# Optimization experiments

Measured on AMD Instinct MI355X. Metric: run time of the kernel, lower is better.

Reference implementation:

```python
import jax, jax.numpy as jnp
import numpy as np

VOCAB = 4823          # round(feature_size_criteo[512])
EMB = 128             # embedding_size
B = 16384             # batch
N_SPARSE = 26
N_DENSE = 13
HID = 256


def setup_inputs() -> dict:
    key = jax.random.key(0)
    ks = jax.random.split(key, 8)
    dense_input = jax.random.normal(ks[0], (B, N_DENSE), dtype=jnp.float32)
    sparse_input = jax.random.randint(ks[1], (B, N_SPARSE), 0, VOCAB, dtype=jnp.int32)
    emb1 = jax.random.normal(ks[2], (VOCAB, 1), dtype=jnp.float32) * 0.02
    emb2 = jax.random.normal(ks[3], (VOCAB, EMB), dtype=jnp.float32) * 0.02
    fm_w = jax.random.normal(ks[4], (1, N_DENSE), dtype=jnp.float32) * 0.1
    w1 = jax.random.normal(ks[5], (HID, N_SPARSE * EMB), dtype=jnp.float32) * (1.0 / np.sqrt(N_SPARSE * EMB))
    w2 = jax.random.normal(ks[6], (HID, HID), dtype=jnp.float32) * (1.0 / np.sqrt(HID))
    w3 = jax.random.normal(ks[7], (1, HID), dtype=jnp.float32) * (1.0 / np.sqrt(HID))
    return {"dense_input": dense_input, "sparse_input": sparse_input,
            "emb1": emb1, "emb2": emb2, "fm_w": fm_w,
            "w1": w1, "w2": w2, "w3": w3}


def reference(dense_input, sparse_input, emb1, emb2, fm_w, w1, w2, w3):
    # first-order FM part
    sparse_1dim = emb1[sparse_input]                     # [B, 26, 1]
    fm_dense = dense_input @ fm_w.T                      # [B, 1]
    fm_sparse = jnp.sum(sparse_1dim, axis=1)             # [B, 1]
    y1 = fm_dense + fm_sparse

    # second-order FM part (sum-square minus square-sum trick)
    sparse_2dim = emb2[sparse_input]                     # [B, 26, EMB]
    s = jnp.sum(sparse_2dim, axis=1)                     # [B, EMB]
    ss = jnp.sum(jnp.square(sparse_2dim), axis=1)        # [B, EMB]
    y2 = 0.5 * jnp.sum(jnp.square(s) - ss, axis=1, keepdims=True)  # [B, 1]

    # deep MLP part
    flat = sparse_2dim.reshape(-1, N_SPARSE * EMB)       # [B, 26*EMB]
    h = jax.nn.relu(flat @ w1.T)
    h = jax.nn.relu(h @ w2.T)
    y3 = h @ w3.T                                        # [B, 1]

    return jax.nn.sigmoid(y1 + y2 + y3)
```

## Files before the change

### kernel.cpp

```cpp
#include <hip/hip_runtime.h>
#include <cstdint>
#include <cstddef>


#define B_ROWS   16384
#define NSPARSE  26
#define NDENSE   13
#define EMBD     128
#define HID      256
#define K1       (NSPARSE*EMBD)
#define VOCAB    4823
#define PAD_V    4864
#define NP       (NSPARSE*HID)

typedef unsigned short ushort_t;
typedef __attribute__((ext_vector_type(8))) short bf16x8;
typedef __attribute__((ext_vector_type(8))) unsigned short ushort8;
typedef __attribute__((ext_vector_type(4))) float f32x4;

__device__ __forceinline__ ushort_t f32_bf16(float x) {
    unsigned u = __builtin_bit_cast(unsigned, x);
    u += 0x7fffu + ((u >> 16) & 1u);
    return (ushort_t)(u >> 16);
}
__device__ __forceinline__ float bf16_f32(ushort_t h) {
    return __builtin_bit_cast(float, ((unsigned)h) << 16);
}

__device__ __forceinline__ void gl2lds16(const void* g, void* l) {
    __builtin_amdgcn_global_load_lds(
        (const __attribute__((address_space(1))) void*)g,
        (__attribute__((address_space(3))) void*)l, 16, 0, 0);
}

__global__ void split_kernel(const float* __restrict__ src,
                             ushort_t* __restrict__ dst, int n4) {
    int i = blockIdx.x * blockDim.x + threadIdx.x;
    if (i >= n4) return;
    float4 x = ((const float4*)src)[i];
    union { ushort_t u[4]; uint2 v; } H;
    float xs[4] = {x.x, x.y, x.z, x.w};
#pragma unroll
    for (int j = 0; j < 4; ++j) H.u[j] = f32_bf16(xs[j]);
    ((uint2*)dst)[i] = H.v;
}

__global__ void splitT_kernel(const float* __restrict__ w1,
                              ushort_t* __restrict__ dst, int n4) {
    int i = blockIdx.x * blockDim.x + threadIdx.x;
    if (i >= n4) return;
    int c    = i & 31;
    int rowp = i >> 5;
    int f = rowp >> 8, h = rowp & 255;
    float4 x = ((const float4*)w1)[h * (K1 / 4) + f * 32 + c];
    union { ushort_t u[4]; uint2 v; } H;
    float xs[4] = {x.x, x.y, x.z, x.w};
#pragma unroll
    for (int j = 0; j < 4; ++j) H.u[j] = f32_bf16(xs[j]);
    ((uint2*)dst)[i] = H.v;
}

template <int KDIM, bool RELU>
__global__ __launch_bounds__(256) void gemm_bf16_kernel(
    const ushort_t* __restrict__ A, const ushort_t* __restrict__ Bm,
    ushort_t* __restrict__ C, int ldc) {
    constexpr int NT = KDIM / 32;
    __shared__ union {
        ushort_t ab[2][2][128 * 32];
        ushort_t t[128 * 128];
    } sm;

    const int tid = threadIdx.x;
    const int bm = blockIdx.x, bn = blockIdx.y;

    auto stage = [&](int buf, int kt) {
#pragma unroll
        for (int j = 0; j < 2; ++j) {
            int s   = j * 256 + tid;
            int row = s >> 2;
            int qd  = (s & 3) ^ (row & 3);
            size_t offA = (size_t)(bm * 128 + row) * KDIM + kt * 32 + qd * 8;
            gl2lds16(A + offA, &sm.ab[buf][0][s * 8]);
            size_t offB = (size_t)(bn * 128 + row) * KDIM + kt * 32 + qd * 8;
            gl2lds16(Bm + offB, &sm.ab[buf][1][s * 8]);
        }
    };

    f32x4 acc[4][4] = {};
    const int l = tid & 63, w = tid >> 6;
    const int wr = w >> 1, wc = w & 1;
    const int lrow = l & 15, lq = l >> 4;
    const int qs = lq ^ (lrow & 3);

    stage(0, 0);
    __syncthreads();
    int buf = 0;
    for (int kt = 0; kt < NT; ++kt) {
        if (kt + 1 < NT) stage(buf ^ 1, kt + 1);
        bf16x8 af[4], bf[4];
#pragma unroll
        for (int m = 0; m < 4; ++m)
            af[m] = *(const bf16x8*)&sm.ab[buf][0][(wr * 64 + m * 16 + lrow) * 32 + qs * 8];
#pragma unroll
        for (int n = 0; n < 4; ++n)
            bf[n] = *(const bf16x8*)&sm.ab[buf][1][(wc * 64 + n * 16 + lrow) * 32 + qs * 8];
#pragma unroll
        for (int m = 0; m < 4; ++m)
#pragma unroll
            for (int n = 0; n < 4; ++n)
                acc[m][n] = __builtin_amdgcn_mfma_f32_16x16x32_bf16(af[m], bf[n], acc[m][n], 0, 0, 0);
        __syncthreads();
        buf ^= 1;
    }

#pragma unroll
    for (int m = 0; m < 4; ++m)
#pragma unroll
        for (int n = 0; n < 4; ++n) {
            int col = wc * 64 + n * 16 + lrow;
#pragma unroll
            for (int r = 0; r < 4; ++r) {
                int row = wr * 64 + m * 16 + lq * 4 + r;
                float v = acc[m][n][r];
                if constexpr (RELU) v = fmaxf(v, 0.f);
                sm.t[row * 128 + col] = f32_bf16(v);
            }
        }
    __syncthreads();
    const int r0 = tid >> 4, c16 = tid & 15;
#pragma unroll
    for (int k = 0; k < 8; ++k) {
        int row = r0 + k * 16;
        ushort8 v8 = *(const ushort8*)&sm.t[row * 128 + c16 * 8];
        *(ushort8*)&C[(size_t)(bm * 128 + row) * ldc + bn * 128 + c16 * 8] = v8;
    }
}

__global__ __launch_bounds__(256) void gather_fm_kernel(
    const ushort_t* __restrict__ Pb, const float* __restrict__ dense,
    const int* __restrict__ sidx, const float* __restrict__ emb1,
    const float* __restrict__ emb2, const float* __restrict__ fm_w,
    ushort_t* __restrict__ h1b, float* __restrict__ y12) {
    int b = blockIdx.x * 4 + (threadIdx.x >> 6);
    int l = threadIdx.x & 63;
    int half = l >> 5, li = l & 31;
    int myI = (l < NSPARSE) ? sidx[b * NSPARSE + l] : 0;

    float acc8[8] = {};
#pragma unroll
    for (int fp = 0; fp < NSPARSE / 2; ++fp) {
        int f = fp * 2 + half;
        int v = __shfl(myI, f, 64);
        ushort8 pv = *(const ushort8*)(Pb + (size_t)v * NP + f * HID + li * 8);
#pragma unroll
        for (int j = 0; j < 8; ++j) acc8[j] += bf16_f32(pv[j]);
    }
    float s0 = 0.f, ss0 = 0.f, s1 = 0.f, ss1 = 0.f;
#pragma unroll
    for (int f = 0; f < NSPARSE; ++f) {
        int v = __shfl(myI, f, 64);
        const float* e = emb2 + (size_t)v * EMBD;
        float e0 = e[l], e1 = e[l + 64];
        s0 += e0; ss0 += e0 * e0;
        s1 += e1; ss1 += e1 * e1;
    }
#pragma unroll
    for (int j = 0; j < 8; ++j) acc8[j] += __shfl_xor(acc8[j], 32, 64);
    if (half == 0) {
        ushort8 o;
#pragma unroll
        for (int j = 0; j < 8; ++j) o[j] = f32_bf16(fmaxf(acc8[j], 0.f));
        *(ushort8*)(h1b + (size_t)b * HID + li * 8) = o;
    }
    float r = 0.5f * ((s0 * s0 - ss0) + (s1 * s1 - ss1));
    if (l < NDENSE)  r += dense[b * NDENSE + l] * fm_w[l];
    if (l < NSPARSE) r += emb1[myI];
#pragma unroll
    for (int o = 32; o; o >>= 1) r += __shfl_xor(r, o, 64);
    if (l == 0) y12[b] = r;
}

__global__ __launch_bounds__(256) void final_kernel(
    const ushort_t* __restrict__ h2b, const float* __restrict__ w3,
    const float* __restrict__ y12, float* __restrict__ out) {
    int b = blockIdx.x * 4 + (threadIdx.x >> 6);
    int lane = threadIdx.x & 63;
    const ushort_t* hr = h2b + (size_t)b * HID;
    float a = bf16_f32(hr[lane])       * w3[lane]
            + bf16_f32(hr[lane + 64])  * w3[lane + 64]
            + bf16_f32(hr[lane + 128]) * w3[lane + 128]
            + bf16_f32(hr[lane + 192]) * w3[lane + 192];
#pragma unroll
    for (int o = 32; o; o >>= 1) a += __shfl_xor(a, o, 64);
    if (lane == 0) {
        float z = y12[b] + a;
        out[b] = 1.f / (1.f + __expf(-z));
    }
}

extern "C" void kernel_launch(void* const* d_in, const int* in_sizes, int n_in,
                              void* d_out, int out_size, void* d_ws, size_t ws_size,
                              hipStream_t stream) {
    const float* dense = (const float*)d_in[0];
    const int*   sidx  = (const int*)d_in[1];
    const float* emb1  = (const float*)d_in[2];
    const float* emb2  = (const float*)d_in[3];
    const float* fm_w  = (const float*)d_in[4];
    const float* w1    = (const float*)d_in[5];
    const float* w2    = (const float*)d_in[6];
    const float* w3    = (const float*)d_in[7];
    float* out = (float*)d_out;

    char* p = (char*)d_ws;
    auto carve = [&](size_t bytes) { void* r = (void*)p; p += (bytes + 255) & ~(size_t)255; return r; };
    ushort_t* e2b = (ushort_t*)carve((size_t)PAD_V * EMBD * 2);
    ushort_t* b1b = (ushort_t*)carve((size_t)NP * EMBD * 2);
    ushort_t* w2b = (ushort_t*)carve((size_t)HID * HID * 2);
    ushort_t* h1b = (ushort_t*)carve((size_t)B_ROWS * HID * 2);
    ushort_t* h2b = (ushort_t*)carve((size_t)B_ROWS * HID * 2);
    float*    y12 = (float*)carve((size_t)B_ROWS * 4);
    ushort_t* Pb  = (ushort_t*)carve((size_t)PAD_V * NP * 2);

    int n4;
    n4 = VOCAB * EMBD / 4;
    split_kernel<<<(n4 + 255) / 256, 256, 0, stream>>>(emb2, e2b, n4);
    n4 = NP * EMBD / 4;
    splitT_kernel<<<(n4 + 255) / 256, 256, 0, stream>>>(w1, b1b, n4);
    n4 = HID * HID / 4;
    split_kernel<<<(n4 + 255) / 256, 256, 0, stream>>>(w2, w2b, n4);

    gemm_bf16_kernel<EMBD, false><<<dim3(PAD_V / 128, NP / 128), 256, 0, stream>>>(
        e2b, b1b, Pb, NP);

    gather_fm_kernel<<<B_ROWS / 4, 256, 0, stream>>>(
        Pb, dense, sidx, emb1, emb2, fm_w, h1b, y12);

    gemm_bf16_kernel<HID, true><<<dim3(B_ROWS / 128, HID / 128), 256, 0, stream>>>(
        h1b, w2b, h2b, HID);

    final_kernel<<<B_ROWS / 4, 256, 0, stream>>>(h2b, w3, y12, out);
}
```

Before: 152.6 us.

## Fuse gather, second MLP layer and output into one kernel; merge prep kernels

After: 139.1 us. -8.9%, faster.

```diff
diff --git a/kernel.cpp b/kernel.cpp
--- a/kernel.cpp
+++ b/kernel.cpp
@@ -33,85 +33,82 @@
         (__attribute__((address_space(3))) void*)l, 16, 0, 0);
 }
 
-__global__ void split_kernel(const float* __restrict__ src,
-                             ushort_t* __restrict__ dst, int n4) {
-    int i = blockIdx.x * blockDim.x + threadIdx.x;
-    if (i >= n4) return;
-    float4 x = ((const float4*)src)[i];
+__global__ __launch_bounds__(256) void prep_kernel(
+    const float* __restrict__ emb2, const float* __restrict__ w1,
+    const float* __restrict__ w2, ushort_t* __restrict__ e2b,
+    ushort_t* __restrict__ b1b, ushort_t* __restrict__ w2b) {
+    constexpr int NA = VOCAB * EMBD / 4;
+    constexpr int NB = NP * EMBD / 4;
+    constexpr int NC = HID * HID / 4;
+    int i = blockIdx.x * 256 + threadIdx.x;
+    float4 x;
+    ushort_t* dst;
+    int di;
+    if (i < NA) {
+        x = ((const float4*)emb2)[i]; dst = e2b; di = i;
+    } else if (i < NA + NB) {
+        int j = i - NA;
+        int c = j & 31, rowp = j >> 5;
+        int f = rowp >> 8, h = rowp & 255;
+        x = ((const float4*)w1)[h * (K1 / 4) + f * 32 + c];
+        dst = b1b; di = j;
+    } else if (i < NA + NB + NC) {
+        int j = i - NA - NB;
+        x = ((const float4*)w2)[j]; dst = w2b; di = j;
+    } else return;
     union { ushort_t u[4]; uint2 v; } H;
     float xs[4] = {x.x, x.y, x.z, x.w};
 #pragma unroll
     for (int j = 0; j < 4; ++j) H.u[j] = f32_bf16(xs[j]);
-    ((uint2*)dst)[i] = H.v;
-}
-
-__global__ void splitT_kernel(const float* __restrict__ w1,
-                              ushort_t* __restrict__ dst, int n4) {
-    int i = blockIdx.x * blockDim.x + threadIdx.x;
-    if (i >= n4) return;
-    int c    = i & 31;
-    int rowp = i >> 5;
-    int f = rowp >> 8, h = rowp & 255;
-    float4 x = ((const float4*)w1)[h * (K1 / 4) + f * 32 + c];
-    union { ushort_t u[4]; uint2 v; } H;
-    float xs[4] = {x.x, x.y, x.z, x.w};
-#pragma unroll
-    for (int j = 0; j < 4; ++j) H.u[j] = f32_bf16(xs[j]);
-    ((uint2*)dst)[i] = H.v;
-}
-
-template <int KDIM, bool RELU>
-__global__ __launch_bounds__(256) void gemm_bf16_kernel(
+    ((uint2*)dst)[di] = H.v;
+}
+
+__global__ __launch_bounds__(256) void gemm_p_kernel(
     const ushort_t* __restrict__ A, const ushort_t* __restrict__ Bm,
-    ushort_t* __restrict__ C, int ldc) {
-    constexpr int NT = KDIM / 32;
+    ushort_t* __restrict__ P2) {
     __shared__ union {
-        ushort_t ab[2][2][128 * 32];
+        struct { ushort_t a[128 * 128]; ushort_t b[128 * 128]; } s;
         ushort_t t[128 * 128];
     } sm;
-
     const int tid = threadIdx.x;
     const int bm = blockIdx.x, bn = blockIdx.y;
-
-    auto stage = [&](int buf, int kt) {
-#pragma unroll
-        for (int j = 0; j < 2; ++j) {
-            int s   = j * 256 + tid;
-            int row = s >> 2;
-            int qd  = (s & 3) ^ (row & 3);
-            size_t offA = (size_t)(bm * 128 + row) * KDIM + kt * 32 + qd * 8;
-            gl2lds16(A + offA, &sm.ab[buf][0][s * 8]);
-            size_t offB = (size_t)(bn * 128 + row) * KDIM + kt * 32 + qd * 8;
-            gl2lds16(Bm + offB, &sm.ab[buf][1][s * 8]);
-        }
-    };
-
+    const int lane = tid & 63, wv = tid >> 6;
+
+#pragma unroll
+    for (int i = 0; i < 8; ++i) {
+        int s = (wv * 8 + i) * 64 + lane;
+        int row = s >> 4, g = s & 15;
+        int gs = g ^ (row & 7);
+        gl2lds16(A  + (size_t)(bm * 128 + row) * EMBD + gs * 8, &sm.s.a[s * 8]);
+        gl2lds16(Bm + (size_t)(bn * 128 + row) * EMBD + gs * 8, &sm.s.b[s * 8]);
+    }
+    __syncthreads();
+
+    const int wr = wv >> 1, wc = wv & 1;
+    const int lrow = lane & 15, lq = lane >> 4;
     f32x4 acc[4][4] = {};
-    const int l = tid & 63, w = tid >> 6;
-    const int wr = w >> 1, wc = w & 1;
-    const int lrow = l & 15, lq = l >> 4;
-    const int qs = lq ^ (lrow & 3);
-
-    stage(0, 0);
-    __syncthreads();
-    int buf = 0;
-    for (int kt = 0; kt < NT; ++kt) {
-        if (kt + 1 < NT) stage(buf ^ 1, kt + 1);
+#pragma unroll
+    for (int ks = 0; ks < 4; ++ks) {
         bf16x8 af[4], bf[4];
 #pragma unroll
-        for (int m = 0; m < 4; ++m)
-            af[m] = *(const bf16x8*)&sm.ab[buf][0][(wr * 64 + m * 16 + lrow) * 32 + qs * 8];
-#pragma unroll
-        for (int n = 0; n < 4; ++n)
-            bf[n] = *(const bf16x8*)&sm.ab[buf][1][(wc * 64 + n * 16 + lrow) * 32 + qs * 8];
+        for (int m = 0; m < 4; ++m) {
+            int row = wr * 64 + m * 16 + lrow;
+            int g = (ks * 4 + lq) ^ (row & 7);
+            af[m] = *(const bf16x8*)&sm.s.a[row * 128 + g * 8];
+        }
+#pragma unroll
+        for (int n = 0; n < 4; ++n) {
+            int row = wc * 64 + n * 16 + lrow;
+            int g = (ks * 4 + lq) ^ (row & 7);
+            bf[n] = *(const bf16x8*)&sm.s.b[row * 128 + g * 8];
+        }
 #pragma unroll
         for (int m = 0; m < 4; ++m)
 #pragma unroll
             for (int n = 0; n < 4; ++n)
                 acc[m][n] = __builtin_amdgcn_mfma_f32_16x16x32_bf16(af[m], bf[n], acc[m][n], 0, 0, 0);
-        __syncthreads();
-        buf ^= 1;
-    }
+    }
+    __syncthreads();
 
 #pragma unroll
     for (int m = 0; m < 4; ++m)
@@ -121,80 +118,109 @@
 #pragma unroll
             for (int r = 0; r < 4; ++r) {
                 int row = wr * 64 + m * 16 + lq * 4 + r;
-                float v = acc[m][n][r];
-                if constexpr (RELU) v = fmaxf(v, 0.f);
-                sm.t[row * 128 + col] = f32_bf16(v);
+                sm.t[row * 128 + col] = f32_bf16(acc[m][n][r]);
             }
         }
     __syncthreads();
+    const int f0 = bn >> 1, half = bn & 1;
     const int r0 = tid >> 4, c16 = tid & 15;
 #pragma unroll
     for (int k = 0; k < 8; ++k) {
         int row = r0 + k * 16;
         ushort8 v8 = *(const ushort8*)&sm.t[row * 128 + c16 * 8];
-        *(ushort8*)&C[(size_t)(bm * 128 + row) * ldc + bn * 128 + c16 * 8] = v8;
-    }
-}
-
-__global__ __launch_bounds__(256) void gather_fm_kernel(
-    const ushort_t* __restrict__ Pb, const float* __restrict__ dense,
+        *(ushort8*)&P2[((size_t)f0 * PAD_V + bm * 128 + row) * HID + half * 128 + c16 * 8] = v8;
+    }
+}
+
+#define H1LD 264
+__global__ __launch_bounds__(256) void mega_kernel(
+    const ushort_t* __restrict__ P2, const ushort_t* __restrict__ e2b,
+    const ushort_t* __restrict__ w2b, const float* __restrict__ dense,
     const int* __restrict__ sidx, const float* __restrict__ emb1,
-    const float* __restrict__ emb2, const float* __restrict__ fm_w,
-    ushort_t* __restrict__ h1b, float* __restrict__ y12) {
-    int b = blockIdx.x * 4 + (threadIdx.x >> 6);
-    int l = threadIdx.x & 63;
-    int half = l >> 5, li = l & 31;
-    int myI = (l < NSPARSE) ? sidx[b * NSPARSE + l] : 0;
-
-    float acc8[8] = {};
-#pragma unroll
-    for (int fp = 0; fp < NSPARSE / 2; ++fp) {
-        int f = fp * 2 + half;
-        int v = __shfl(myI, f, 64);
-        ushort8 pv = *(const ushort8*)(Pb + (size_t)v * NP + f * HID + li * 8);
-#pragma unroll
-        for (int j = 0; j < 8; ++j) acc8[j] += bf16_f32(pv[j]);
-    }
-    float s0 = 0.f, ss0 = 0.f, s1 = 0.f, ss1 = 0.f;
-#pragma unroll
+    const float* __restrict__ fm_w, const float* __restrict__ w3,
+    float* __restrict__ out) {
+    __shared__ int      sI[16 * NSPARSE];
+    __shared__ ushort_t h1s[16 * H1LD];
+    __shared__ float    y12s[16];
+    __shared__ float    y3s[4][16];
+
+    const int tid = threadIdx.x;
+    const int b0 = blockIdx.x * 16;
+    for (int i = tid; i < 16 * NSPARSE; i += 256) sI[i] = sidx[b0 * NSPARSE + i];
+    __syncthreads();
+
+    const int row = tid >> 4, h16 = tid & 15;
+    float hacc[16] = {};
+    float s8[8] = {};
+    float ss = 0.f;
+#pragma unroll 4
     for (int f = 0; f < NSPARSE; ++f) {
-        int v = __shfl(myI, f, 64);
-        const float* e = emb2 + (size_t)v * EMBD;
-        float e0 = e[l], e1 = e[l + 64];
-        s0 += e0; ss0 += e0 * e0;
-        s1 += e1; ss1 += e1 * e1;
-    }
-#pragma unroll
-    for (int j = 0; j < 8; ++j) acc8[j] += __shfl_xor(acc8[j], 32, 64);
-    if (half == 0) {
-        ushort8 o;
-#pragma unroll
-        for (int j = 0; j < 8; ++j) o[j] = f32_bf16(fmaxf(acc8[j], 0.f));
-        *(ushort8*)(h1b + (size_t)b * HID + li * 8) = o;
-    }
-    float r = 0.5f * ((s0 * s0 - ss0) + (s1 * s1 - ss1));
-    if (l < NDENSE)  r += dense[b * NDENSE + l] * fm_w[l];
-    if (l < NSPARSE) r += emb1[myI];
-#pragma unroll
-    for (int o = 32; o; o >>= 1) r += __shfl_xor(r, o, 64);
-    if (l == 0) y12[b] = r;
-}
-
-__global__ __launch_bounds__(256) void final_kernel(
-    const ushort_t* __restrict__ h2b, const float* __restrict__ w3,
-    const float* __restrict__ y12, float* __restrict__ out) {
-    int b = blockIdx.x * 4 + (threadIdx.x >> 6);
-    int lane = threadIdx.x & 63;
-    const ushort_t* hr = h2b + (size_t)b * HID;
-    float a = bf16_f32(hr[lane])       * w3[lane]
-            + bf16_f32(hr[lane + 64])  * w3[lane + 64]
-            + bf16_f32(hr[lane + 128]) * w3[lane + 128]
-            + bf16_f32(hr[lane + 192]) * w3[lane + 192];
-#pragma unroll
-    for (int o = 32; o; o >>= 1) a += __shfl_xor(a, o, 64);
-    if (lane == 0) {
-        float z = y12[b] + a;
-        out[b] = 1.f / (1.f + __expf(-z));
+        int v = sI[row * NSPARSE + f];
+        const ushort_t* pp = P2 + ((size_t)f * PAD_V + v) * HID + h16 * 16;
+        ushort8 p0 = *(const ushort8*)pp;
+        ushort8 p1 = *(const ushort8*)(pp + 8);
+        ushort8 ev = *(const ushort8*)(e2b + (size_t)v * EMBD + h16 * 8);
+#pragma unroll
+        for (int j = 0; j < 8; ++j) {
+            hacc[j]     += bf16_f32(p0[j]);
+            hacc[8 + j] += bf16_f32(p1[j]);
+            float e = bf16_f32(ev[j]);
+            s8[j] += e; ss += e * e;
+        }
+    }
+    {
+        union { ushort_t u[8]; ushort8 v; } o0, o1;
+#pragma unroll
+        for (int j = 0; j < 8; ++j) {
+            o0.u[j] = f32_bf16(fmaxf(hacc[j], 0.f));
+            o1.u[j] = f32_bf16(fmaxf(hacc[8 + j], 0.f));
+        }
+        *(ushort8*)&h1s[row * H1LD + h16 * 16]     = o0.v;
+        *(ushort8*)&h1s[row * H1LD + h16 * 16 + 8] = o1.v;
+    }
+    float part = 0.f;
+#pragma unroll
+    for (int j = 0; j < 8; ++j) part += s8[j] * s8[j];
+    part = 0.5f * (part - ss);
+    if (h16 < NDENSE) {
+        part += dense[(b0 + row) * NDENSE + h16] * fm_w[h16];
+        part += emb1[sI[row * NSPARSE + h16]] + emb1[sI[row * NSPARSE + 13 + h16]];
+    }
+#pragma unroll
+    for (int o = 8; o; o >>= 1) part += __shfl_xor(part, o, 64);
+    if (h16 == 0) y12s[row] = part;
+    __syncthreads();
+
+    const int lane = tid & 63, wv = tid >> 6;
+    const int lrow = lane & 15, lq = lane >> 4;
+    f32x4 acc[4] = {};
+#pragma unroll
+    for (int ks = 0; ks < 8; ++ks) {
+        bf16x8 af = *(const bf16x8*)&h1s[lrow * H1LD + ks * 32 + lq * 8];
+#pragma unroll
+        for (int nt = 0; nt < 4; ++nt) {
+            bf16x8 bf = *(const bf16x8*)&w2b[(size_t)(wv * 64 + nt * 16 + lrow) * HID + ks * 32 + lq * 8];
+            acc[nt] = __builtin_amdgcn_mfma_f32_16x16x32_bf16(af, bf, acc[nt], 0, 0, 0);
+        }
+    }
+    float y3p[4] = {};
+#pragma unroll
+    for (int nt = 0; nt < 4; ++nt) {
+        float wv3 = w3[wv * 64 + nt * 16 + lrow];
+#pragma unroll
+        for (int r = 0; r < 4; ++r) y3p[r] += fmaxf(acc[nt][r], 0.f) * wv3;
+    }
+#pragma unroll
+    for (int r = 0; r < 4; ++r)
+#pragma unroll
+        for (int o = 8; o; o >>= 1) y3p[r] += __shfl_xor(y3p[r], o, 64);
+    if (lrow == 0)
+#pragma unroll
+        for (int r = 0; r < 4; ++r) y3s[wv][lq * 4 + r] = y3p[r];
+    __syncthreads();
+    if (tid < 16) {
+        float z = y12s[tid] + y3s[0][tid] + y3s[1][tid] + y3s[2][tid] + y3s[3][tid];
+        out[b0 + tid] = 1.f / (1.f + __expf(-z));
     }
 }
 
@@ -216,27 +242,13 @@
     ushort_t* e2b = (ushort_t*)carve((size_t)PAD_V * EMBD * 2);
     ushort_t* b1b = (ushort_t*)carve((size_t)NP * EMBD * 2);
     ushort_t* w2b = (ushort_t*)carve((size_t)HID * HID * 2);
-    ushort_t* h1b = (ushort_t*)carve((size_t)B_ROWS * HID * 2);
-    ushort_t* h2b = (ushort_t*)carve((size_t)B_ROWS * HID * 2);
-    float*    y12 = (float*)carve((size_t)B_ROWS * 4);
-    ushort_t* Pb  = (ushort_t*)carve((size_t)PAD_V * NP * 2);
-
-    int n4;
-    n4 = VOCAB * EMBD / 4;
-    split_kernel<<<(n4 + 255) / 256, 256, 0, stream>>>(emb2, e2b, n4);
-    n4 = NP * EMBD / 4;
-    splitT_kernel<<<(n4 + 255) / 256, 256, 0, stream>>>(w1, b1b, n4);
-    n4 = HID * HID / 4;
-    split_kernel<<<(n4 + 255) / 256, 256, 0, stream>>>(w2, w2b, n4);
-
-    gemm_bf16_kernel<EMBD, false><<<dim3(PAD_V / 128, NP / 128), 256, 0, stream>>>(
-        e2b, b1b, Pb, NP);
-
-    gather_fm_kernel<<<B_ROWS / 4, 256, 0, stream>>>(
-        Pb, dense, sidx, emb1, emb2, fm_w, h1b, y12);
-
-    gemm_bf16_kernel<HID, true><<<dim3(B_ROWS / 128, HID / 128), 256, 0, stream>>>(
-        h1b, w2b, h2b, HID);
-
-    final_kernel<<<B_ROWS / 4, 256, 0, stream>>>(h2b, w3, y12, out);
-}
+    ushort_t* P2  = (ushort_t*)carve((size_t)NSPARSE * PAD_V * HID * 2);
+
+    constexpr int NPREP = (VOCAB * EMBD + NP * EMBD + HID * HID) / 4;
+    prep_kernel<<<(NPREP + 255) / 256, 256, 0, stream>>>(emb2, w1, w2, e2b, b1b, w2b);
+
+    gemm_p_kernel<<<dim3(PAD_V / 128, NP / 128), 256, 0, stream>>>(e2b, b1b, P2);
+
+    mega_kernel<<<B_ROWS / 16, 256, 0, stream>>>(
+        P2, e2b, w2b, dense, sidx, emb1, fm_w, w3, out);
+}
```
